# Kernel tuning notes

Hardware: AMD Instinct MI355X
Metric: run time of the kernel (lower is better)

The kernel has to match this reference:

```python
import jax, jax.numpy as jnp
import numpy as np

N_NODES = 100000
N_EDGES = 1600000
D_IN = 128
D_OUT = 128


def setup_inputs() -> dict:
    key = jax.random.key(0)
    k1, k2, k3, k4, k5 = jax.random.split(key, 5)
    x = jax.random.normal(k1, (N_NODES, D_IN), dtype=jnp.float32)
    weight = jax.random.normal(k2, (D_IN, D_OUT), dtype=jnp.float32)
    edge_src = jax.random.randint(k3, (N_EDGES,), 0, N_NODES, dtype=jnp.int32)
    edge_dst = jax.random.randint(k4, (N_EDGES,), 0, N_NODES, dtype=jnp.int32)
    edge_val = jax.random.uniform(k5, (N_EDGES,), dtype=jnp.float32)
    return {"x": x, "weight": weight, "edge_src": edge_src,
            "edge_dst": edge_dst, "edge_val": edge_val}


def reference(x, weight, edge_src, edge_dst, edge_val):
    # SpMM: T[dst] += val * x[src]   (adjacency @ features)
    msgs = x[edge_src] * edge_val[:, None]              # [E, D_IN]
    T = jax.ops.segment_sum(msgs, edge_dst, num_segments=N_NODES)  # [N, D_IN]
    # Dense projection: Z = T @ W
    Z = T @ weight                                      # [N, D_OUT]
    return Z
```

## Files before the change

kernel.cpp:

```cpp
#include <hip/hip_runtime.h>

#define N_NODES 100000
#define N_EDGES 1600000
#define D 128
#define CAP 48

#define NBUCK 391
#define BUCKCAP 5120
#define LBCAP 19

typedef __attribute__((ext_vector_type(8))) short bf16x8;
typedef __attribute__((ext_vector_type(4))) float f32x4;
typedef __attribute__((ext_vector_type(2))) float f32x2;
typedef unsigned short ushort_t;
typedef unsigned long long u64;

__device__ __forceinline__ ushort_t bf(float f) {
    unsigned u = __float_as_uint(f);
    return (ushort_t)((u + 0x7fffu + ((u >> 16) & 1u)) >> 16);
}

__global__ __launch_bounds__(256) void setup_kernel(int* __restrict__ bcnt,
                                                    const float* __restrict__ W,
                                                    ushort_t* __restrict__ Wt) {
    int b = blockIdx.x;
    if (b == 64) {
        for (int i = threadIdx.x; i < NBUCK; i += 256) bcnt[i] = 0;
    } else {
        int i = b * 256 + threadIdx.x;
        int n = i >> 7, k = i & 127;
        Wt[i] = bf(W[k * D + n]);
    }
}

#define BIN_BLOCKS 391
__global__ __launch_bounds__(1024) void bin_kernel(
        const int* __restrict__ src, const int* __restrict__ dst,
        const float* __restrict__ val,
        u64* __restrict__ gbuck, int* __restrict__ bcnt) {
    __shared__ u64 lbuf[NBUCK][LBCAP];
    __shared__ int lcnt[NBUCK];
    __shared__ int lbase[NBUCK];
    const int tid = threadIdx.x;
    for (int i = tid; i < NBUCK; i += 1024) lcnt[i] = 0;
    __syncthreads();

    const int base = blockIdx.x * 4096 + tid;
    u64 pk[4]; int bk[4], ok[4], slot[4];
#pragma unroll
    for (int j = 0; j < 4; ++j) {
        int e = base + j * 1024;
        ok[j] = (e < N_EDGES);
        int d = 0, s = 0; float v = 0.f;
        if (ok[j]) { d = dst[e]; s = src[e]; v = val[e]; }
        unsigned q = (unsigned)(v * 32767.0f + 0.5f);
        pk[j] = (u64)(unsigned)s | ((u64)(unsigned)d << 17) | ((u64)q << 34);
        bk[j] = d >> 8;
    }
#pragma unroll
    for (int j = 0; j < 4; ++j) {
        slot[j] = ok[j] ? atomicAdd(&lcnt[bk[j]], 1) : LBCAP;
        if (ok[j] && slot[j] < LBCAP) lbuf[bk[j]][slot[j]] = pk[j];
    }
    __syncthreads();
    for (int b = tid; b < NBUCK; b += 1024) {
        int c = lcnt[b]; c = (c < LBCAP) ? c : LBCAP;
        lbase[b] = atomicAdd(&bcnt[b], c);
    }
    __syncthreads();
    for (int i = tid; i < NBUCK * LBCAP; i += 1024) {
        int b = i / LBCAP, el = i - b * LBCAP;
        int c = lcnt[b]; c = (c < LBCAP) ? c : LBCAP;
        if (el < c) {
            int gb = lbase[b] + el;
            if (gb < BUCKCAP) gbuck[(long long)b * BUCKCAP + gb] = lbuf[b][el];
        }
    }
#pragma unroll
    for (int j = 0; j < 4; ++j)
        if (ok[j] && slot[j] >= LBCAP) {
            int gb = atomicAdd(&bcnt[bk[j]], 1);
            if (gb < BUCKCAP) gbuck[(long long)bk[j] * BUCKCAP + gb] = pk[j];
        }
}

__global__ __launch_bounds__(256) void scatter_kernel(
        const u64* __restrict__ gbuck, const int* __restrict__ bcnt,
        int* __restrict__ cnt, unsigned* __restrict__ epack) {
    __shared__ unsigned ep_l[256 * CAP];
    __shared__ int cnt_l[256];
    const int b = blockIdx.x;
    const int tid = threadIdx.x;
    cnt_l[tid] = 0;
    __syncthreads();

    int total = bcnt[b]; total = (total < BUCKCAP) ? total : BUCKCAP;
    const u64* bp = gbuck + (long long)b * BUCKCAP;
    for (int i = tid; i < total; i += 256) {
        u64 p = bp[i];
        int dloc = (int)(p >> 17) & 255;
        int slot = atomicAdd(&cnt_l[dloc], 1);
        if (slot < CAP)
            ep_l[dloc * CAP + slot] =
                (unsigned)(p & 0x1ffff) | ((unsigned)(p >> 34) << 17);
    }
    __syncthreads();

    const int node0 = b * 256;
    int nvalid = N_NODES - node0; nvalid = (nvalid < 256) ? nvalid : 256;
    for (int i = tid; i < nvalid * CAP; i += 256)
        epack[(long long)node0 * CAP + i] = ep_l[i];
    if (tid < nvalid) {
        int c = cnt_l[tid]; c = (c < CAP) ? c : CAP;
        cnt[node0 + tid] = c;
    }
}

#define GEMM_BLOCKS 1563
#define LP (D + 8)
__global__ __launch_bounds__(256) void gemm_kernel(
        const float* __restrict__ X, const ushort_t* __restrict__ Wt,
        ushort_t* __restrict__ Y) {
    __shared__ ushort_t lx[64][LP];
    __shared__ ushort_t lw[D][LP];
    const int tid = threadIdx.x;
    const long long row0 = (long long)blockIdx.x * 64;

#pragma unroll
    for (int it = 0; it < 8; ++it) {
        int c = tid + it * 256;
        int r = c >> 4, c16 = c & 15;
        *(ulonglong2*)&lw[r][c16 * 8] = *(const ulonglong2*)(Wt + r * D + c16 * 8);
    }
#pragma unroll
    for (int it = 0; it < 8; ++it) {
        int c = tid + it * 256;
        int r = c >> 5, c4 = c & 31;
        long long gr = row0 + r;
        if (gr >= N_NODES) gr = 0;
        float4 v = *(const float4*)(X + gr * D + c4 * 4);
        ushort4 b4 = make_ushort4(bf(v.x), bf(v.y), bf(v.z), bf(v.w));
        *(ushort4*)&lx[r][c4 * 4] = b4;
    }
    __syncthreads();

    const int wave = tid >> 6, lane = tid & 63;
    const int mrow = lane & 15, quad = lane >> 4;

    f32x4 acc[8];
#pragma unroll
    for (int nt = 0; nt < 8; ++nt) acc[nt] = (f32x4){0.f, 0.f, 0.f, 0.f};

#pragma unroll
    for (int kc = 0; kc < 4; ++kc) {
        bf16x8 a = *(const bf16x8*)&lx[wave * 16 + mrow][kc * 32 + quad * 8];
#pragma unroll
        for (int nt = 0; nt < 8; ++nt) {
            bf16x8 bfr = *(const bf16x8*)&lw[nt * 16 + mrow][kc * 32 + quad * 8];
            acc[nt] = __builtin_amdgcn_mfma_f32_16x16x32_bf16(a, bfr, acc[nt], 0, 0, 0);
        }
    }

    const long long baserow = row0 + wave * 16 + quad * 4;
#pragma unroll
    for (int nt = 0; nt < 8; ++nt)
#pragma unroll
        for (int r = 0; r < 4; ++r) {
            long long grow = baserow + r;
            if (grow < N_NODES)
                Y[grow * D + nt * 16 + mrow] = bf(acc[nt][r]);
        }
}

__global__ __launch_bounds__(256) void gather_kernel(
        const unsigned* __restrict__ Yu, const int* __restrict__ cnt,
        const unsigned* __restrict__ epack, float* __restrict__ Z) {
    const int n = __builtin_amdgcn_readfirstlane(blockIdx.x * 4 + (threadIdx.x >> 6));
    const int lane = threadIdx.x & 63;

    int c = cnt[n];
    c = (c < CAP) ? c : CAP;
    c = __builtin_amdgcn_readfirstlane(c);
    const unsigned* __restrict__ ep = epack + n * CAP;
    float ax = 0.f, ay = 0.f;
    const float q2f = 1.0f / 32767.0f;

    for (int e = 0; e < c; e += 16) {
        unsigned p[16];
#pragma unroll
        for (int j = 0; j < 16; ++j) {
            int idx = e + j;
            idx = (idx < c) ? idx : (c - 1);
            p[j] = ep[idx];
        }
#pragma unroll
        for (int j = 0; j < 16; ++j) {
            unsigned q = (e + j < c) ? (p[j] >> 17) : 0u;
            unsigned y = Yu[((p[j] & 0x1ffffu) << 6) + lane];
            float v = (float)q * q2f;
            ax += v * __uint_as_float(y << 16);
            ay += v * __uint_as_float(y & 0xffff0000u);
        }
    }

    f32x2 r; r[0] = ax; r[1] = ay;
    __builtin_nontemporal_store(r, (f32x2*)Z + (long long)n * 64 + lane);
}

extern "C" void kernel_launch(void* const* d_in, const int* in_sizes, int n_in,
                              void* d_out, int out_size, void* d_ws, size_t ws_size,
                              hipStream_t stream) {
    const float* x    = (const float*)d_in[0];
    const float* W    = (const float*)d_in[1];
    const int*   esrc = (const int*)  d_in[2];
    const int*   edst = (const int*)  d_in[3];
    const float* eval_= (const float*)d_in[4];
    float*       Z    = (float*)d_out;

    char* w = (char*)d_ws;
    int*      cnt   = (int*)     (w + 0);
    unsigned* epack = (unsigned*)(w + 400000);
    ushort_t* Wt    = (ushort_t*)(w + 19600000);
    ushort_t* Yu    = (ushort_t*)(w + 19632768);
    u64*      gbuck = (u64*)     (w + 19632768);
    int*      bcnt  = (int*)     (w + 45228672);

    setup_kernel<<<65, 256, 0, stream>>>(bcnt, W, Wt);
    bin_kernel<<<BIN_BLOCKS, 1024, 0, stream>>>(esrc, edst, eval_, gbuck, bcnt);
    scatter_kernel<<<NBUCK, 256, 0, stream>>>(gbuck, bcnt, cnt, epack);
    gemm_kernel<<<GEMM_BLOCKS, 256, 0, stream>>>(x, Wt, Yu);
    gather_kernel<<<N_NODES / 4, 256, 0, stream>>>((const unsigned*)Yu, cnt, epack, Z);
}
```

Baseline: 203.8 us.

## Fuse per-node edge bucketing into gather kernel, drop scatter pass

Removes the separate scatter kernel that built a per-node CSR-like edge list in global memory. The gather kernel now reads the coarse bucket directly, filters the edges belonging to its 64 nodes into shared memory, then accumulates. This saves one launch and the epack/cnt global write and read. In exchange, each bucket is read four times, once by each of the four blocks that share it, and most of those reads are filtered out. Each wave also now processes 16 nodes serially instead of one node per wave.

Result: no change. 204.5 us (+0.4%).

```diff
diff --git a/kernel.cpp b/kernel.cpp
--- a/kernel.cpp
+++ b/kernel.cpp
@@ -8,6 +8,7 @@
 #define NBUCK 391
 #define BUCKCAP 5120
 #define LBCAP 19
+#define GF_BLOCKS 1563
 
 typedef __attribute__((ext_vector_type(8))) short bf16x8;
 typedef __attribute__((ext_vector_type(4))) float f32x4;
@@ -84,38 +85,6 @@
         }
 }
 
-__global__ __launch_bounds__(256) void scatter_kernel(
-        const u64* __restrict__ gbuck, const int* __restrict__ bcnt,
-        int* __restrict__ cnt, unsigned* __restrict__ epack) {
-    __shared__ unsigned ep_l[256 * CAP];
-    __shared__ int cnt_l[256];
-    const int b = blockIdx.x;
-    const int tid = threadIdx.x;
-    cnt_l[tid] = 0;
-    __syncthreads();
-
-    int total = bcnt[b]; total = (total < BUCKCAP) ? total : BUCKCAP;
-    const u64* bp = gbuck + (long long)b * BUCKCAP;
-    for (int i = tid; i < total; i += 256) {
-        u64 p = bp[i];
-        int dloc = (int)(p >> 17) & 255;
-        int slot = atomicAdd(&cnt_l[dloc], 1);
-        if (slot < CAP)
-            ep_l[dloc * CAP + slot] =
-                (unsigned)(p & 0x1ffff) | ((unsigned)(p >> 34) << 17);
-    }
-    __syncthreads();
-
-    const int node0 = b * 256;
-    int nvalid = N_NODES - node0; nvalid = (nvalid < 256) ? nvalid : 256;
-    for (int i = tid; i < nvalid * CAP; i += 256)
-        epack[(long long)node0 * CAP + i] = ep_l[i];
-    if (tid < nvalid) {
-        int c = cnt_l[tid]; c = (c < CAP) ? c : CAP;
-        cnt[node0 + tid] = c;
-    }
-}
-
 #define GEMM_BLOCKS 1563
 #define LP (D + 8)
 __global__ __launch_bounds__(256) void gemm_kernel(
@@ -172,39 +141,65 @@
         }
 }
 
-__global__ __launch_bounds__(256) void gather_kernel(
-        const unsigned* __restrict__ Yu, const int* __restrict__ cnt,
-        const unsigned* __restrict__ epack, float* __restrict__ Z) {
-    const int n = __builtin_amdgcn_readfirstlane(blockIdx.x * 4 + (threadIdx.x >> 6));
-    const int lane = threadIdx.x & 63;
-
-    int c = cnt[n];
-    c = (c < CAP) ? c : CAP;
-    c = __builtin_amdgcn_readfirstlane(c);
-    const unsigned* __restrict__ ep = epack + n * CAP;
-    float ax = 0.f, ay = 0.f;
+__global__ __launch_bounds__(256) void gather_fused(
+        const u64* __restrict__ gbuck, const int* __restrict__ bcnt,
+        const unsigned* __restrict__ Yu, float* __restrict__ Z) {
+    __shared__ unsigned ep_l[64 * CAP];
+    __shared__ int cnt_l[64];
+    const int b = blockIdx.x;
+    const int tid = threadIdx.x;
+    if (tid < 64) cnt_l[tid] = 0;
+    __syncthreads();
+
+    const int cb = b >> 2;
+    int total = bcnt[cb]; total = (total < BUCKCAP) ? total : BUCKCAP;
+    const u64* bp = gbuck + (long long)cb * BUCKCAP;
+    for (int i = tid; i < total; i += 256) {
+        u64 p = bp[i];
+        int d = (int)((p >> 17) & 0x1ffff);
+        if ((d >> 6) == b) {
+            int dloc = d & 63;
+            int slot = atomicAdd(&cnt_l[dloc], 1);
+            if (slot < CAP)
+                ep_l[dloc * CAP + slot] =
+                    (unsigned)(p & 0x1ffff) | ((unsigned)(p >> 34) << 17);
+        }
+    }
+    __syncthreads();
+
+    const int wave = tid >> 6, lane = tid & 63;
     const float q2f = 1.0f / 32767.0f;
-
-    for (int e = 0; e < c; e += 16) {
-        unsigned p[16];
-#pragma unroll
-        for (int j = 0; j < 16; ++j) {
-            int idx = e + j;
-            idx = (idx < c) ? idx : (c - 1);
-            p[j] = ep[idx];
-        }
-#pragma unroll
-        for (int j = 0; j < 16; ++j) {
-            unsigned q = (e + j < c) ? (p[j] >> 17) : 0u;
-            unsigned y = Yu[((p[j] & 0x1ffffu) << 6) + lane];
-            float v = (float)q * q2f;
-            ax += v * __uint_as_float(y << 16);
-            ay += v * __uint_as_float(y & 0xffff0000u);
-        }
-    }
-
-    f32x2 r; r[0] = ax; r[1] = ay;
-    __builtin_nontemporal_store(r, (f32x2*)Z + (long long)n * 64 + lane);
+#pragma unroll 1
+    for (int t = 0; t < 16; ++t) {
+        const int nloc = wave * 16 + t;
+        const int n = b * 64 + nloc;
+        if (n >= N_NODES) break;
+        int c = cnt_l[nloc];
+        c = (c < CAP) ? c : CAP;
+        c = __builtin_amdgcn_readfirstlane(c);
+        const unsigned* ep = &ep_l[nloc * CAP];
+        float ax = 0.f, ay = 0.f;
+
+        for (int e = 0; e < c; e += 16) {
+            unsigned p[16];
+#pragma unroll
+            for (int j = 0; j < 16; ++j) {
+                int idx = e + j;
+                idx = (idx < c) ? idx : (c - 1);
+                p[j] = ep[idx];
+            }
+#pragma unroll
+            for (int j = 0; j < 16; ++j) {
+                unsigned q = (e + j < c) ? (p[j] >> 17) : 0u;
+                unsigned y = Yu[((p[j] & 0x1ffffu) << 6) + lane];
+                float v = (float)q * q2f;
+                ax += v * __uint_as_float(y << 16);
+                ay += v * __uint_as_float(y & 0xffff0000u);
+            }
+        }
+        f32x2 r; r[0] = ax; r[1] = ay;
+        __builtin_nontemporal_store(r, (f32x2*)Z + (long long)n * 64 + lane);
+    }
 }
 
 extern "C" void kernel_launch(void* const* d_in, const int* in_sizes, int n_in,
@@ -218,16 +213,13 @@
     float*       Z    = (float*)d_out;
 
     char* w = (char*)d_ws;
-    int*      cnt   = (int*)     (w + 0);
-    unsigned* epack = (unsigned*)(w + 400000);
-    ushort_t* Wt    = (ushort_t*)(w + 19600000);
-    ushort_t* Yu    = (ushort_t*)(w + 19632768);
-    u64*      gbuck = (u64*)     (w + 19632768);
-    int*      bcnt  = (int*)     (w + 45228672);
+    ushort_t* Wt    = (ushort_t*)(w + 0);
+    ushort_t* Yu    = (ushort_t*)(w + 32768);
+    u64*      gbuck = (u64*)     (w + 25632768);
+    int*      bcnt  = (int*)     (w + 41648128);
 
     setup_kernel<<<65, 256, 0, stream>>>(bcnt, W, Wt);
     bin_kernel<<<BIN_BLOCKS, 1024, 0, stream>>>(esrc, edst, eval_, gbuck, bcnt);
-    scatter_kernel<<<NBUCK, 256, 0, stream>>>(gbuck, bcnt, cnt, epack);
     gemm_kernel<<<GEMM_BLOCKS, 256, 0, stream>>>(x, Wt, Yu);
-    gather_kernel<<<N_NODES / 4, 256, 0, stream>>>((const unsigned*)Yu, cnt, epack, Z);
-}
+    gather_fused<<<GF_BLOCKS, 256, 0, stream>>>(gbuck, bcnt, (const unsigned*)Yu, Z);
+}
```

## Replace LDS-staged edge binning with per-sub-bucket global atomics and overflow list

Applied to the files above, without the earlier changes.

The bin kernel drops its shared-memory staging buffers and block-level flush. Each edge now does a global atomicAdd directly into one of 8 sub-buckets per destination bucket, chosen by block index, to spread atomic contention. Sub-buckets that overflow spill into a small global overflow list, which every scatter block scans in full. This removes LDS usage and barriers and allows smaller blocks with higher occupancy, but it issues one global atomic per edge instead of one per bucket per block.

New measurement: 338.9 us. +66.3%, slower.

```diff
diff --git a/kernel.cpp b/kernel.cpp
--- a/kernel.cpp
+++ b/kernel.cpp
@@ -6,8 +6,8 @@
 #define CAP 48
 
 #define NBUCK 391
-#define BUCKCAP 5120
-#define LBCAP 19
+#define SUBCAP 704
+#define OVFCAP 4096
 
 typedef __attribute__((ext_vector_type(8))) short bf16x8;
 typedef __attribute__((ext_vector_type(4))) float f32x4;
@@ -25,7 +25,7 @@
                                                     ushort_t* __restrict__ Wt) {
     int b = blockIdx.x;
     if (b == 64) {
-        for (int i = threadIdx.x; i < NBUCK; i += 256) bcnt[i] = 0;
+        for (int i = threadIdx.x; i < NBUCK * 8 + 1; i += 256) bcnt[i] = 0;
     } else {
         int i = b * 256 + threadIdx.x;
         int n = i >> 7, k = i & 127;
@@ -33,59 +33,37 @@
     }
 }
 
-#define BIN_BLOCKS 391
-__global__ __launch_bounds__(1024) void bin_kernel(
+#define BIN_BLOCKS 1563
+__global__ __launch_bounds__(256) void bin_kernel(
         const int* __restrict__ src, const int* __restrict__ dst,
         const float* __restrict__ val,
-        u64* __restrict__ gbuck, int* __restrict__ bcnt) {
-    __shared__ u64 lbuf[NBUCK][LBCAP];
-    __shared__ int lcnt[NBUCK];
-    __shared__ int lbase[NBUCK];
-    const int tid = threadIdx.x;
-    for (int i = tid; i < NBUCK; i += 1024) lcnt[i] = 0;
-    __syncthreads();
-
-    const int base = blockIdx.x * 4096 + tid;
-    u64 pk[4]; int bk[4], ok[4], slot[4];
+        u64* __restrict__ gbuck, int* __restrict__ bcnt,
+        u64* __restrict__ ovf, int* __restrict__ ovfcnt) {
+    const int sub = blockIdx.x & 7;
+    const int base = blockIdx.x * 1024 + threadIdx.x;
 #pragma unroll
     for (int j = 0; j < 4; ++j) {
-        int e = base + j * 1024;
-        ok[j] = (e < N_EDGES);
-        int d = 0, s = 0; float v = 0.f;
-        if (ok[j]) { d = dst[e]; s = src[e]; v = val[e]; }
-        unsigned q = (unsigned)(v * 32767.0f + 0.5f);
-        pk[j] = (u64)(unsigned)s | ((u64)(unsigned)d << 17) | ((u64)q << 34);
-        bk[j] = d >> 8;
-    }
-#pragma unroll
-    for (int j = 0; j < 4; ++j) {
-        slot[j] = ok[j] ? atomicAdd(&lcnt[bk[j]], 1) : LBCAP;
-        if (ok[j] && slot[j] < LBCAP) lbuf[bk[j]][slot[j]] = pk[j];
-    }
-    __syncthreads();
-    for (int b = tid; b < NBUCK; b += 1024) {
-        int c = lcnt[b]; c = (c < LBCAP) ? c : LBCAP;
-        lbase[b] = atomicAdd(&bcnt[b], c);
-    }
-    __syncthreads();
-    for (int i = tid; i < NBUCK * LBCAP; i += 1024) {
-        int b = i / LBCAP, el = i - b * LBCAP;
-        int c = lcnt[b]; c = (c < LBCAP) ? c : LBCAP;
-        if (el < c) {
-            int gb = lbase[b] + el;
-            if (gb < BUCKCAP) gbuck[(long long)b * BUCKCAP + gb] = lbuf[b][el];
-        }
-    }
-#pragma unroll
-    for (int j = 0; j < 4; ++j)
-        if (ok[j] && slot[j] >= LBCAP) {
-            int gb = atomicAdd(&bcnt[bk[j]], 1);
-            if (gb < BUCKCAP) gbuck[(long long)bk[j] * BUCKCAP + gb] = pk[j];
-        }
+        int e = base + j * 256;
+        if (e < N_EDGES) {
+            int d = dst[e], s = src[e];
+            float v = val[e];
+            unsigned q = (unsigned)(v * 32767.0f + 0.5f);
+            u64 pk = (u64)(unsigned)s | ((u64)(unsigned)d << 17) | ((u64)q << 34);
+            int cell = (d >> 8) * 8 + sub;
+            int idx = atomicAdd(&bcnt[cell], 1);
+            if (idx >= 0 && idx < SUBCAP)
+                gbuck[(long long)cell * SUBCAP + idx] = pk;
+            else {
+                int o = atomicAdd(ovfcnt, 1);
+                if (o >= 0 && o < OVFCAP) ovf[o] = pk;
+            }
+        }
+    }
 }
 
 __global__ __launch_bounds__(256) void scatter_kernel(
         const u64* __restrict__ gbuck, const int* __restrict__ bcnt,
+        const u64* __restrict__ ovf, const int* __restrict__ ovfcnt,
         int* __restrict__ cnt, unsigned* __restrict__ epack) {
     __shared__ unsigned ep_l[256 * CAP];
     __shared__ int cnt_l[256];
@@ -94,15 +72,31 @@
     cnt_l[tid] = 0;
     __syncthreads();
 
-    int total = bcnt[b]; total = (total < BUCKCAP) ? total : BUCKCAP;
-    const u64* bp = gbuck + (long long)b * BUCKCAP;
-    for (int i = tid; i < total; i += 256) {
-        u64 p = bp[i];
-        int dloc = (int)(p >> 17) & 255;
-        int slot = atomicAdd(&cnt_l[dloc], 1);
-        if (slot < CAP)
-            ep_l[dloc * CAP + slot] =
-                (unsigned)(p & 0x1ffff) | ((unsigned)(p >> 34) << 17);
+#pragma unroll 1
+    for (int s = 0; s < 8; ++s) {
+        int c = bcnt[b * 8 + s];
+        c = (c < 0) ? 0 : c; c = (c < SUBCAP) ? c : SUBCAP;
+        const u64* bp = gbuck + (long long)(b * 8 + s) * SUBCAP;
+        for (int i = tid; i < c; i += 256) {
+            u64 p = bp[i];
+            int dloc = (int)(p >> 17) & 255;
+            int slot = atomicAdd(&cnt_l[dloc], 1);
+            if (slot < CAP)
+                ep_l[dloc * CAP + slot] =
+                    (unsigned)(p & 0x1ffff) | ((unsigned)(p >> 34) << 17);
+        }
+    }
+    int oc = *ovfcnt;
+    oc = (oc < 0) ? 0 : oc; oc = (oc < OVFCAP) ? oc : OVFCAP;
+    for (int i = tid; i < oc; i += 256) {
+        u64 p = ovf[i];
+        int d = (int)((p >> 17) & 0x1ffff);
+        if ((d >> 8) == b) {
+            int slot = atomicAdd(&cnt_l[d & 255], 1);
+            if (slot < CAP)
+                ep_l[(d & 255) * CAP + slot] =
+                    (unsigned)(p & 0x1ffff) | ((unsigned)(p >> 34) << 17);
+        }
     }
     __syncthreads();
 
@@ -218,16 +212,19 @@
     float*       Z    = (float*)d_out;
 
     char* w = (char*)d_ws;
-    int*      cnt   = (int*)     (w + 0);
-    unsigned* epack = (unsigned*)(w + 400000);
-    ushort_t* Wt    = (ushort_t*)(w + 19600000);
-    ushort_t* Yu    = (ushort_t*)(w + 19632768);
-    u64*      gbuck = (u64*)     (w + 19632768);
-    int*      bcnt  = (int*)     (w + 45228672);
+    int*      cnt    = (int*)     (w + 0);
+    unsigned* epack  = (unsigned*)(w + 400000);
+    ushort_t* Wt     = (ushort_t*)(w + 19600000);
+    ushort_t* Yu     = (ushort_t*)(w + 19632768);
+    u64*      gbuck  = (u64*)     (w + 19632768);
+    int*      bcnt   = (int*)     (w + 37249664);
+    int*      ovfcnt = bcnt + NBUCK * 8;
+    u64*      ovf    = (u64*)     (w + 37262184);
 
     setup_kernel<<<65, 256, 0, stream>>>(bcnt, W, Wt);
-    bin_kernel<<<BIN_BLOCKS, 1024, 0, stream>>>(esrc, edst, eval_, gbuck, bcnt);
-    scatter_kernel<<<NBUCK, 256, 0, stream>>>(gbuck, bcnt, cnt, epack);
+    bin_kernel<<<BIN_BLOCKS, 256, 0, stream>>>(esrc, edst, eval_, gbuck, bcnt,
+                                               ovf, ovfcnt);
+    scatter_kernel<<<NBUCK, 256, 0, stream>>>(gbuck, bcnt, ovf, ovfcnt, cnt, epack);
     gemm_kernel<<<GEMM_BLOCKS, 256, 0, stream>>>(x, Wt, Yu);
     gather_kernel<<<N_NODES / 4, 256, 0, stream>>>((const unsigned*)Yu, cnt, epack, Z);
 }
```
